# Kernel optimization log

Hardware: AMD Instinct MI355X
Metric: run time of the kernel (lower is better)

## Reference

```python
import jax, jax.numpy as jnp
import numpy as np

HEADS = 16
NEG = -1e9  # matches masked_fill(-1000000000.0)

def setup_inputs() -> dict:
    key = jax.random.key(0)
    ks = jax.random.split(key, 7)
    B, T, C = 2, 2048, 1024
    s = 1.0 / np.sqrt(C)
    return {
        "q": jax.random.normal(ks[0], (B, T, C), jnp.float32),
        "k": jax.random.normal(ks[1], (B, T, C), jnp.float32),
        "v": jax.random.normal(ks[2], (B, T, C), jnp.float32),
        "Wq": jax.random.normal(ks[3], (C, C), jnp.float32) * s,
        "Wk": jax.random.normal(ks[4], (C, C), jnp.float32) * s,
        "Wv": jax.random.normal(ks[5], (C, C), jnp.float32) * s,
        "Wo": jax.random.normal(ks[6], (C, C), jnp.float32) * s,
    }

def reference(q, k, v, Wq, Wk, Wv, Wo):
    B, T, C = q.shape
    h = HEADS
    dk = C // h
    # torch Linear (no bias): y = x @ W.T ; weight is [out, in]
    def proj(x, W):
        return (x @ W.T).reshape(B, T, h, dk).transpose(0, 2, 1, 3)  # [B,h,T,dk]
    qh, kh, vh = proj(q, Wq), proj(k, Wk), proj(v, Wv)
    scale = jnp.asarray(dk, q.dtype) ** 0.5
    scores = jnp.einsum('bhqd,bhkd->bhqk', qh / scale, kh)  # [B,h,T,T]
    causal = jnp.tril(jnp.ones((T, T), dtype=bool))
    scores = jnp.where(causal[None, None], scores, jnp.asarray(NEG, scores.dtype))
    attn = jax.nn.softmax(scores, axis=-1)
    out = jnp.einsum('bhqk,bhkd->bhqd', attn, vh)  # [B,h,T,dk]
    concat = out.transpose(0, 2, 1, 3).reshape(B, T, C)
    return concat @ Wo.T
```

## Files before the change

kernel.cpp:

```cpp
#include <hip/hip_runtime.h>
#include <hip/hip_bf16.h>

typedef __bf16 bf16x8 __attribute__((ext_vector_type(8)));
typedef float  f32x4  __attribute__((ext_vector_type(4)));
typedef unsigned short u16;

__device__ __forceinline__ u16 f2bf(float f) {
    __bf16 h = (__bf16)f;
    return __builtin_bit_cast(u16, h);
}

__device__ __forceinline__ f32x4 mfma16(bf16x8 a, bf16x8 b, f32x4 c) {
    return __builtin_amdgcn_mfma_f32_16x16x32_bf16(a, b, c, 0, 0, 0);
}

__device__ __forceinline__ bf16x8 cvt8(float4 a0, float4 a1) {
    bf16x8 u;
    u[0] = (__bf16)a0.x; u[1] = (__bf16)a0.y; u[2] = (__bf16)a0.z; u[3] = (__bf16)a0.w;
    u[4] = (__bf16)a1.x; u[5] = (__bf16)a1.y; u[6] = (__bf16)a1.z; u[7] = (__bf16)a1.w;
    return u;
}

__global__ __launch_bounds__(256) void cvtW(const float* __restrict__ W0,
                                            const float* __restrict__ W1,
                                            const float* __restrict__ W2,
                                            const float* __restrict__ W3,
                                            u16* __restrict__ dst) {
    const int t     = blockIdx.x * 256 + threadIdx.x;
    const int which = t >> 17;
    const int off   = (t & 0x1FFFF) * 8;
    const float* s  = (which == 0) ? W0 : (which == 1) ? W1 : (which == 2) ? W2 : W3;
    float4 f0 = *(const float4*)(s + off);
    float4 f1 = *(const float4*)(s + off + 4);
    *(bf16x8*)(dst + ((size_t)which << 20) + off) = cvt8(f0, f1);
}

__global__ __launch_bounds__(256) void gemm_qkv(const float* __restrict__ q,
                                                const float* __restrict__ k,
                                                const float* __restrict__ v,
                                                const u16* __restrict__ Wb,
                                                u16* __restrict__ Qp,
                                                u16* __restrict__ Kp,
                                                u16* __restrict__ Vt) {
    constexpr int K = 1024, N = 1024;
    __shared__ __align__(16) u16 As[2][4096];
    __shared__ __align__(16) u16 Bs[2][4096];

    const int tid  = threadIdx.x;
    const int lane = tid & 63;
    const int w    = tid >> 6;
    const int wr = w >> 1, wc = w & 1;
    const int wg    = (blockIdx.x & 7) * 96 + (blockIdx.x >> 3);
    const int which = wg >> 8;
    const int inner = wg & 255;
    const int m0 = (inner >> 3) * 128, n0 = (inner & 7) * 128;
    const int colg = lane & 15, rowg = lane >> 4;

    const float* A = (which == 0) ? q : (which == 1) ? k : v;
    const u16*   W = Wb + ((size_t)which << 20);

    size_t aoff[2], boff[2];
    int wio[2];
#pragma unroll
    for (int i = 0; i < 2; ++i) {
        const int c   = i * 256 + tid;
        const int row = c >> 2;
        const int kc  = c & 3;
        aoff[i] = (size_t)(m0 + row) * K + kc * 8;
        boff[i] = (size_t)(n0 + row) * K + kc * 8;
        const int kcs = kc ^ ((row >> 1) & 3);
        wio[i] = row * 32 + kcs * 8;
    }
    const int kcr   = rowg ^ ((colg >> 1) & 3);
    const int rbase = colg * 32 + kcr * 8;

    f32x4 acc[4][4];
#pragma unroll
    for (int i = 0; i < 4; ++i)
#pragma unroll
        for (int j = 0; j < 4; ++j) acc[i][j] = (f32x4){0.f, 0.f, 0.f, 0.f};

    float4 a0[2], a1[2];
    uint4  bv[2];
#pragma unroll
    for (int i = 0; i < 2; ++i) {
        a0[i] = *(const float4*)(A + aoff[i]);
        a1[i] = *(const float4*)(A + aoff[i] + 4);
        bv[i] = *(const uint4*)(W + boff[i]);
    }
#pragma unroll
    for (int i = 0; i < 2; ++i) {
        *(bf16x8*)(&As[0][wio[i]]) = cvt8(a0[i], a1[i]);
        *(uint4*)(&Bs[0][wio[i]]) = bv[i];
    }
    __syncthreads();

    int p = 0;
    for (int t = 0; t < 32; ++t) {
        if (t < 31) {
            const int kk = (t + 1) * 32;
#pragma unroll
            for (int i = 0; i < 2; ++i) {
                a0[i] = *(const float4*)(A + aoff[i] + kk);
                a1[i] = *(const float4*)(A + aoff[i] + kk + 4);
                bv[i] = *(const uint4*)(W + boff[i] + kk);
            }
        }
        {
            bf16x8 af[4], bfr[4];
#pragma unroll
            for (int mi = 0; mi < 4; ++mi)
                af[mi] = *(const bf16x8*)(&As[p][(wr * 64 + mi * 16) * 32 + rbase]);
#pragma unroll
            for (int ni = 0; ni < 4; ++ni)
                bfr[ni] = *(const bf16x8*)(&Bs[p][(wc * 64 + ni * 16) * 32 + rbase]);
#pragma unroll
            for (int mi = 0; mi < 4; ++mi)
#pragma unroll
                for (int ni = 0; ni < 4; ++ni)
                    acc[mi][ni] = mfma16(af[mi], bfr[ni], acc[mi][ni]);
        }
        if (t < 31) {
#pragma unroll
            for (int i = 0; i < 2; ++i) {
                *(bf16x8*)(&As[p ^ 1][wio[i]]) = cvt8(a0[i], a1[i]);
                *(uint4*)(&Bs[p ^ 1][wio[i]]) = bv[i];
            }
        }
        __syncthreads();
        p ^= 1;
    }

    u16* Crm = (which == 0) ? Qp : Kp;
#pragma unroll
    for (int mi = 0; mi < 4; ++mi) {
#pragma unroll
        for (int ni = 0; ni < 4; ++ni) {
#pragma unroll
            for (int r = 0; r < 4; ++r) {
                const int row = m0 + wr * 64 + mi * 16 + rowg * 4 + r;
                const int col = n0 + wc * 64 + ni * 16 + colg;
                const float vv = acc[mi][ni][r];
                if (which < 2) {
                    Crm[(size_t)row * N + col] = f2bf(vv);
                } else {
                    const int b = row >> 11, tt = row & 2047;
                    const int h = col >> 6,  d = col & 63;
                    Vt[((size_t)((b * 16 + h) * 64 + d) << 11) + tt] = f2bf(vv);
                }
            }
        }
    }
}

__global__ __launch_bounds__(256) void gemm_out(const u16* __restrict__ Ap,
                                                const u16* __restrict__ W,
                                                float* __restrict__ Cp) {
    constexpr int K = 1024, N = 1024;
    __shared__ __align__(16) u16 As[2][2048];
    __shared__ __align__(16) u16 Bs[2][4096];

    const int tid  = threadIdx.x;
    const int lane = tid & 63;
    const int w    = tid >> 6;
    const int wr = w >> 1, wc = w & 1;
    const int wg = (blockIdx.x & 7) * 64 + (blockIdx.x >> 3);
    const int m0 = (wg >> 3) * 64, n0 = (wg & 7) * 128;
    const int colg = lane & 15, rowg = lane >> 4;

    const int rowA = tid >> 2, kcA = tid & 3;
    const size_t aoff = (size_t)(m0 + rowA) * K + kcA * 8;
    const int wiA = rowA * 32 + (kcA ^ ((rowA >> 1) & 3)) * 8;

    size_t boff[2];
    int wiB[2];
#pragma unroll
    for (int i = 0; i < 2; ++i) {
        const int c   = i * 256 + tid;
        const int row = c >> 2;
        const int kc  = c & 3;
        boff[i] = (size_t)(n0 + row) * K + kc * 8;
        wiB[i] = row * 32 + (kc ^ ((row >> 1) & 3)) * 8;
    }
    const int kcr   = rowg ^ ((colg >> 1) & 3);
    const int rbase = colg * 32 + kcr * 8;

    f32x4 acc[2][4];
#pragma unroll
    for (int i = 0; i < 2; ++i)
#pragma unroll
        for (int j = 0; j < 4; ++j) acc[i][j] = (f32x4){0.f, 0.f, 0.f, 0.f};

    uint4 av = *(const uint4*)(Ap + aoff);
    uint4 bv[2];
#pragma unroll
    for (int i = 0; i < 2; ++i) bv[i] = *(const uint4*)(W + boff[i]);
    *(uint4*)(&As[0][wiA]) = av;
#pragma unroll
    for (int i = 0; i < 2; ++i) *(uint4*)(&Bs[0][wiB[i]]) = bv[i];
    __syncthreads();

    int p = 0;
    for (int t = 0; t < 32; ++t) {
        if (t < 31) {
            const int kk = (t + 1) * 32;
            av = *(const uint4*)(Ap + aoff + kk);
#pragma unroll
            for (int i = 0; i < 2; ++i) bv[i] = *(const uint4*)(W + boff[i] + kk);
        }
        {
            bf16x8 af[2], bfr[4];
#pragma unroll
            for (int mi = 0; mi < 2; ++mi)
                af[mi] = *(const bf16x8*)(&As[p][(wr * 32 + mi * 16) * 32 + rbase]);
#pragma unroll
            for (int ni = 0; ni < 4; ++ni)
                bfr[ni] = *(const bf16x8*)(&Bs[p][(wc * 64 + ni * 16) * 32 + rbase]);
#pragma unroll
            for (int mi = 0; mi < 2; ++mi)
#pragma unroll
                for (int ni = 0; ni < 4; ++ni)
                    acc[mi][ni] = mfma16(af[mi], bfr[ni], acc[mi][ni]);
        }
        if (t < 31) {
            *(uint4*)(&As[p ^ 1][wiA]) = av;
#pragma unroll
            for (int i = 0; i < 2; ++i) *(uint4*)(&Bs[p ^ 1][wiB[i]]) = bv[i];
        }
        __syncthreads();
        p ^= 1;
    }

#pragma unroll
    for (int mi = 0; mi < 2; ++mi)
#pragma unroll
        for (int ni = 0; ni < 4; ++ni)
#pragma unroll
            for (int r = 0; r < 4; ++r) {
                const int row = m0 + wr * 32 + mi * 16 + rowg * 4 + r;
                const int col = n0 + wc * 64 + ni * 16 + colg;
                Cp[(size_t)row * N + col] = acc[mi][ni][r];
            }
}

constexpr float CEXP = 0.18033688011112042f;

__global__ __launch_bounds__(256) void attn_causal(const u16* __restrict__ Qp,
                                                   const u16* __restrict__ Kp,
                                                   const u16* __restrict__ Vt,
                                                   u16* __restrict__ concat) {
    constexpr int T = 2048, C = 1024;
    __shared__ __align__(16) u16 Ks[128 * 64];
    __shared__ __align__(16) u16 Vs[64 * 128];
    __shared__ __align__(16) u16 Pl[4][2048];

    const int tid  = threadIdx.x;
    const int lane = tid & 63;
    const int w    = tid >> 6;
    const int colg = lane & 15, rowg = lane >> 4;

    const int idx = blockIdx.x;
    const int xcd = idx & 7;
    const int i1  = idx >> 3;
    const int bh  = xcd * 4 + (i1 & 3);
    const int qg  = 31 - (i1 >> 2);
    const int b = bh >> 4, h = bh & 15;

    const int q0 = (qg * 4 + w) * 16;
    const int nt    = (q0 + 143) >> 7;
    const int ktmax = ((qg * 4 + 3) * 16 + 143) >> 7;

    const char* Kg = (const char*)(Kp + (size_t)(b * T) * C + h * 64);
    const char* Vg = (const char*)(Vt + ((size_t)(b * 16 + h) * 64) * T);
    char* Ksb = (char*)Ks;
    char* Vsb = (char*)Vs;
    char* Pw  = (char*)&Pl[w][0];

    const u16* Qb = Qp + (size_t)(b * T + q0 + colg) * C + h * 64;
    const bf16x8 qf0 = *(const bf16x8*)(Qb + rowg * 8);
    const bf16x8 qf1 = *(const bf16x8*)(Qb + 32 + rowg * 8);

    float mm = -1e30f, ll = 0.f;
    f32x4 O[4];
#pragma unroll
    for (int g = 0; g < 4; ++g) O[g] = (f32x4){0.f, 0.f, 0.f, 0.f};

    const int sw = (colg & 7) << 4;

    for (int kt = 0; kt < ktmax; ++kt) {
        const int kvb = kt * 128;
        uint4 kst[4], vst[4];
#pragma unroll
        for (int i2 = 0; i2 < 4; ++i2) {
            const int s  = i2 * 4096 + tid * 16;
            const int kv = s >> 7, ir = s & 127;
            kst[i2] = *(const uint4*)(Kg + (size_t)(kvb + kv) * 2048 + ir);
            const int d = s >> 8, irv = s & 255;
            vst[i2] = *(const uint4*)(Vg + (size_t)d * 4096 + (size_t)kvb * 2 + irv);
        }
#pragma unroll
        for (int i2 = 0; i2 < 4; ++i2) {
            const int s  = i2 * 4096 + tid * 16;
            const int kv = s >> 7;
            *(uint4*)(Ksb + (s ^ ((kv & 7) << 4))) = kst[i2];
            const int d = s >> 8;
            *(uint4*)(Vsb + (s ^ ((d & 7) << 4))) = vst[i2];
        }
        __syncthreads();

        if (kt < nt) {
            float pr[8][4];
#pragma unroll
            for (int sub = 0; sub < 8; ++sub) {
                const int kb = (sub * 16 + colg) * 128 + rowg * 16;
                bf16x8 kf0 = *(const bf16x8*)(Ksb + (kb ^ sw));
                bf16x8 kf1 = *(const bf16x8*)(Ksb + ((kb + 64) ^ sw));
                f32x4 t = (f32x4){0.f, 0.f, 0.f, 0.f};
                t = mfma16(kf0, qf0, t);
                t = mfma16(kf1, qf1, t);
#pragma unroll
                for (int r = 0; r < 4; ++r) pr[sub][r] = t[r];
            }
            if (kvb + 127 > q0) {
#pragma unroll
                for (int sub = 0; sub < 8; ++sub)
#pragma unroll
                    for (int r = 0; r < 4; ++r)
                        if (kvb + sub * 16 + rowg * 4 + r > q0 + colg) pr[sub][r] = -1e30f;
            }
            float mx[8];
#pragma unroll
            for (int sub = 0; sub < 8; ++sub)
                mx[sub] = fmaxf(fmaxf(pr[sub][0], pr[sub][1]), fmaxf(pr[sub][2], pr[sub][3]));
            float pm = fmaxf(fmaxf(fmaxf(mx[0], mx[1]), fmaxf(mx[2], mx[3])),
                             fmaxf(fmaxf(mx[4], mx[5]), fmaxf(mx[6], mx[7])));
            pm = fmaxf(pm, __shfl_xor(pm, 16, 64));
            pm = fmaxf(pm, __shfl_xor(pm, 32, 64));
            if (__any(pm > mm + 40.f)) {
                const float mn = fmaxf(mm, pm);
                const float sc = __builtin_amdgcn_exp2f((mm - mn) * CEXP);
                mm = mn;
                ll *= sc;
#pragma unroll
                for (int r = 0; r < 4; ++r) {
                    const float scr = __shfl(sc, (lane & 48) + rowg * 4 + r, 64);
#pragma unroll
                    for (int g = 0; g < 4; ++g) O[g][r] *= scr;
                }
            }
            float rs = 0.f;
#pragma unroll
            for (int sub = 0; sub < 8; ++sub) {
                const float e0 = __builtin_amdgcn_exp2f((pr[sub][0] - mm) * CEXP);
                const float e1 = __builtin_amdgcn_exp2f((pr[sub][1] - mm) * CEXP);
                const float e2 = __builtin_amdgcn_exp2f((pr[sub][2] - mm) * CEXP);
                const float e3 = __builtin_amdgcn_exp2f((pr[sub][3] - mm) * CEXP);
                pr[sub][0] = e0; pr[sub][1] = e1; pr[sub][2] = e2; pr[sub][3] = e3;
                rs += (e0 + e1) + (e2 + e3);
            }
            rs += __shfl_xor(rs, 16, 64);
            rs += __shfl_xor(rs, 32, 64);
            ll += rs;
#pragma unroll
            for (int sub = 0; sub < 8; ++sub) {
                uint2 pk;
                pk.x = (unsigned)f2bf(pr[sub][0]) | ((unsigned)f2bf(pr[sub][1]) << 16);
                pk.y = (unsigned)f2bf(pr[sub][2]) | ((unsigned)f2bf(pr[sub][3]) << 16);
                const int wb = (colg * 256 + sub * 32 + rowg * 8) ^ sw;
                *(uint2*)(Pw + wb) = pk;
            }
            bf16x8 pf[4];
#pragma unroll
            for (int kc = 0; kc < 4; ++kc)
                pf[kc] = *(const bf16x8*)(Pw + ((colg * 256 + kc * 64 + rowg * 16) ^ sw));
#pragma unroll
            for (int g = 0; g < 4; ++g) {
                const int vb0 = (g * 16 + colg) * 256 + rowg * 16;
#pragma unroll
                for (int kc = 0; kc < 4; ++kc) {
                    bf16x8 vf = *(const bf16x8*)(Vsb + ((vb0 + kc * 64) ^ sw));
                    O[g] = mfma16(pf[kc], vf, O[g]);
                }
            }
        }
        __syncthreads();
    }

#pragma unroll
    for (int r = 0; r < 4; ++r) {
        const float lr = __shfl(ll, (lane & 48) + rowg * 4 + r, 64);
        const float rc = 1.f / lr;
        const size_t base = (size_t)(b * T + q0 + rowg * 4 + r) * C + h * 64;
#pragma unroll
        for (int g = 0; g < 4; ++g)
            concat[base + g * 16 + colg] = f2bf(O[g][r] * rc);
    }
}

extern "C" void kernel_launch(void* const* d_in, const int* in_sizes, int n_in,
                              void* d_out, int out_size, void* d_ws, size_t ws_size,
                              hipStream_t stream) {
    const float* q  = (const float*)d_in[0];
    const float* k  = (const float*)d_in[1];
    const float* v  = (const float*)d_in[2];
    const float* Wq = (const float*)d_in[3];
    const float* Wk = (const float*)d_in[4];
    const float* Wv = (const float*)d_in[5];
    const float* Wo = (const float*)d_in[6];
    float* out = (float*)d_out;

    constexpr size_t NELEM = (size_t)4096 * 1024;
    constexpr size_t WSZ   = (size_t)1 << 20;
    u16* Wbf = (u16*)d_ws;
    u16* Qp  = Wbf + 4 * WSZ;
    u16* Kp  = Qp + NELEM;
    u16* Vt  = Kp + NELEM;
    u16* Cc  = Vt + NELEM;

    cvtW<<<2048, 256, 0, stream>>>(Wq, Wk, Wv, Wo, Wbf);

    gemm_qkv<<<768, 256, 0, stream>>>(q, k, v, Wbf, Qp, Kp, Vt);

    attn_causal<<<1024, 256, 0, stream>>>(Qp, Kp, Vt, Cc);

    gemm_out<<<512, 256, 0, stream>>>(Cc, Wbf + 3 * WSZ, out);
}
```

Before: 134.4 us.

## Use 512-thread blocks with single-buffered LDS in QKV projection GEMM

The QKV projection GEMM now runs 8 waves per block instead of 4, with each wave computing a 64x32 sub-tile, so each thread holds half as many accumulators. Register double-buffering and the two LDS buffers are replaced by one LDS buffer and a load-store-sync-compute-sync loop. The aim is higher occupancy and lower register and LDS pressure per block. The cost is that global-load latency is no longer overlapped with MFMA inside a block, and there are now two barriers per K step.

```diff
diff --git a/kernel.cpp b/kernel.cpp
--- a/kernel.cpp
+++ b/kernel.cpp
@@ -35,21 +35,21 @@
     *(bf16x8*)(dst + ((size_t)which << 20) + off) = cvt8(f0, f1);
 }
 
-__global__ __launch_bounds__(256) void gemm_qkv(const float* __restrict__ q,
-                                                const float* __restrict__ k,
-                                                const float* __restrict__ v,
-                                                const u16* __restrict__ Wb,
-                                                u16* __restrict__ Qp,
-                                                u16* __restrict__ Kp,
-                                                u16* __restrict__ Vt) {
+__global__ __launch_bounds__(512, 6) void gemm_qkv(const float* __restrict__ q,
+                                                   const float* __restrict__ k,
+                                                   const float* __restrict__ v,
+                                                   const u16* __restrict__ Wb,
+                                                   u16* __restrict__ Qp,
+                                                   u16* __restrict__ Kp,
+                                                   u16* __restrict__ Vt) {
     constexpr int K = 1024, N = 1024;
-    __shared__ __align__(16) u16 As[2][4096];
-    __shared__ __align__(16) u16 Bs[2][4096];
+    __shared__ __align__(16) u16 As[4096];
+    __shared__ __align__(16) u16 Bs[4096];
 
     const int tid  = threadIdx.x;
     const int lane = tid & 63;
     const int w    = tid >> 6;
-    const int wr = w >> 1, wc = w & 1;
+    const int wr = w >> 2, wc = w & 3;
     const int wg    = (blockIdx.x & 7) * 96 + (blockIdx.x >> 3);
     const int which = wg >> 8;
     const int inner = wg & 255;
@@ -59,87 +59,53 @@
     const float* A = (which == 0) ? q : (which == 1) ? k : v;
     const u16*   W = Wb + ((size_t)which << 20);
 
-    size_t aoff[2], boff[2];
-    int wio[2];
-#pragma unroll
-    for (int i = 0; i < 2; ++i) {
-        const int c   = i * 256 + tid;
-        const int row = c >> 2;
-        const int kc  = c & 3;
-        aoff[i] = (size_t)(m0 + row) * K + kc * 8;
-        boff[i] = (size_t)(n0 + row) * K + kc * 8;
-        const int kcs = kc ^ ((row >> 1) & 3);
-        wio[i] = row * 32 + kcs * 8;
-    }
+    const int rowS = tid >> 2, kcS = tid & 3;
+    const size_t aoff = (size_t)(m0 + rowS) * K + kcS * 8;
+    const size_t boff = (size_t)(n0 + rowS) * K + kcS * 8;
+    const int wio = rowS * 32 + (kcS ^ ((rowS >> 1) & 3)) * 8;
+
     const int kcr   = rowg ^ ((colg >> 1) & 3);
     const int rbase = colg * 32 + kcr * 8;
 
-    f32x4 acc[4][4];
+    f32x4 acc[4][2];
 #pragma unroll
     for (int i = 0; i < 4; ++i)
 #pragma unroll
-        for (int j = 0; j < 4; ++j) acc[i][j] = (f32x4){0.f, 0.f, 0.f, 0.f};
-
-    float4 a0[2], a1[2];
-    uint4  bv[2];
-#pragma unroll
-    for (int i = 0; i < 2; ++i) {
-        a0[i] = *(const float4*)(A + aoff[i]);
-        a1[i] = *(const float4*)(A + aoff[i] + 4);
-        bv[i] = *(const uint4*)(W + boff[i]);
-    }
-#pragma unroll
-    for (int i = 0; i < 2; ++i) {
-        *(bf16x8*)(&As[0][wio[i]]) = cvt8(a0[i], a1[i]);
-        *(uint4*)(&Bs[0][wio[i]]) = bv[i];
-    }
-    __syncthreads();
-
-    int p = 0;
+        for (int j = 0; j < 2; ++j) acc[i][j] = (f32x4){0.f, 0.f, 0.f, 0.f};
+
     for (int t = 0; t < 32; ++t) {
-        if (t < 31) {
-            const int kk = (t + 1) * 32;
-#pragma unroll
-            for (int i = 0; i < 2; ++i) {
-                a0[i] = *(const float4*)(A + aoff[i] + kk);
-                a1[i] = *(const float4*)(A + aoff[i] + kk + 4);
-                bv[i] = *(const uint4*)(W + boff[i] + kk);
-            }
-        }
-        {
-            bf16x8 af[4], bfr[4];
-#pragma unroll
-            for (int mi = 0; mi < 4; ++mi)
-                af[mi] = *(const bf16x8*)(&As[p][(wr * 64 + mi * 16) * 32 + rbase]);
-#pragma unroll
-            for (int ni = 0; ni < 4; ++ni)
-                bfr[ni] = *(const bf16x8*)(&Bs[p][(wc * 64 + ni * 16) * 32 + rbase]);
-#pragma unroll
-            for (int mi = 0; mi < 4; ++mi)
-#pragma unroll
-                for (int ni = 0; ni < 4; ++ni)
-                    acc[mi][ni] = mfma16(af[mi], bfr[ni], acc[mi][ni]);
-        }
-        if (t < 31) {
-#pragma unroll
-            for (int i = 0; i < 2; ++i) {
-                *(bf16x8*)(&As[p ^ 1][wio[i]]) = cvt8(a0[i], a1[i]);
-                *(uint4*)(&Bs[p ^ 1][wio[i]]) = bv[i];
-            }
-        }
-        __syncthreads();
-        p ^= 1;
+        const int kk = t * 32;
+        float4 a0 = *(const float4*)(A + aoff + kk);
+        float4 a1 = *(const float4*)(A + aoff + kk + 4);
+        uint4  bv = *(const uint4*)(W + boff + kk);
+        *(bf16x8*)(&As[wio]) = cvt8(a0, a1);
+        *(uint4*)(&Bs[wio]) = bv;
+        __syncthreads();
+
+        bf16x8 af[4], bfr[2];
+#pragma unroll
+        for (int mi = 0; mi < 4; ++mi)
+            af[mi] = *(const bf16x8*)(&As[(wr * 64 + mi * 16) * 32 + rbase]);
+#pragma unroll
+        for (int ni = 0; ni < 2; ++ni)
+            bfr[ni] = *(const bf16x8*)(&Bs[(wc * 32 + ni * 16) * 32 + rbase]);
+#pragma unroll
+        for (int mi = 0; mi < 4; ++mi)
+#pragma unroll
+            for (int ni = 0; ni < 2; ++ni)
+                acc[mi][ni] = mfma16(af[mi], bfr[ni], acc[mi][ni]);
+        __syncthreads();
     }
 
     u16* Crm = (which == 0) ? Qp : Kp;
 #pragma unroll
     for (int mi = 0; mi < 4; ++mi) {
 #pragma unroll
-        for (int ni = 0; ni < 4; ++ni) {
+        for (int ni = 0; ni < 2; ++ni) {
 #pragma unroll
             for (int r = 0; r < 4; ++r) {
                 const int row = m0 + wr * 64 + mi * 16 + rowg * 4 + r;
-                const int col = n0 + wc * 64 + ni * 16 + colg;
+                const int col = n0 + wc * 32 + ni * 16 + colg;
                 const float vv = acc[mi][ni][r];
                 if (which < 2) {
                     Crm[(size_t)row * N + col] = f2bf(vv);
@@ -419,7 +385,7 @@
 
     cvtW<<<2048, 256, 0, stream>>>(Wq, Wk, Wv, Wo, Wbf);
 
-    gemm_qkv<<<768, 256, 0, stream>>>(q, k, v, Wbf, Qp, Kp, Vt);
+    gemm_qkv<<<768, 512, 0, stream>>>(q, k, v, Wbf, Qp, Kp, Vt);
 
     attn_causal<<<1024, 256, 0, stream>>>(Qp, Kp, Vt, Cc);
 
```

New measurement: 132.0 us. Within noise of the previous version (-1.8%).
